# Kernel tuning notes

Hardware: AMD Instinct MI355X
Metric: run time of the kernel (lower is better)

## Reference

```python
import jax, jax.numpy as jnp
import numpy as np

KS = 5          # B-spline kernel_size per pseudo-coordinate dim
DIM = 2         # pseudo-coordinate dimensionality
NUM_GRAPHS = 64


def spline_conv(x, src, dst, edge_attr, W, root, bias):
    """Degree-1 open B-spline conv (torch-spline-conv semantics, aggr='mean').
    x: [N,Cin], edge_attr: [E,DIM] in [0,1], W: [KS**DIM,Cin,Cout]."""
    N = x.shape[0]
    E = src.shape[0]
    v = edge_attr * (KS - 1)                                   # [E,DIM]
    k_lo = jnp.clip(jnp.floor(v), 0, KS - 2).astype(jnp.int32) # lower knot index
    frac = v - k_lo.astype(v.dtype)                            # [E,DIM]
    # Precompute x @ W_k for all K kernel weights per node: [N,K,Cout]
    xW = jnp.einsum('nc,kco->nko', x, W)
    msg = jnp.zeros((E, W.shape[2]), x.dtype)
    # 2^DIM = 4 nonzero basis products for degree-1 splines
    for bits in ((0, 0), (0, 1), (1, 0), (1, 1)):
        b = jnp.ones((E,), x.dtype)
        wi = jnp.zeros((E,), jnp.int32)
        stride = 1
        for d, bit in enumerate(bits):
            b = b * (frac[:, d] if bit else (1.0 - frac[:, d]))
            wi = wi + (k_lo[:, d] + bit) * stride
            stride *= KS
        msg = msg + b[:, None] * xW[src, wi]                   # gather [E,Cout]
    agg = jax.ops.segment_sum(msg, dst, num_segments=N)
    deg = jax.ops.segment_sum(jnp.ones((E,), x.dtype), dst, num_segments=N)
    agg = agg / jnp.maximum(deg, 1.0)[:, None]                 # mean aggregation
    return agg + x @ root + bias


def setup_inputs() -> dict:
    key = jax.random.key(0)
    ks = jax.random.split(key, 12)
    N, E = 20000, 320000
    Cin, H, O = 1, 32, 10
    K = KS * KS
    p = lambda k, s: jax.random.normal(k, s, jnp.float32) * 0.1
    return {
        'x': jax.random.normal(ks[0], (N, Cin), jnp.float32),
        'edge_attr': jax.random.uniform(ks[1], (E, DIM), jnp.float32),
        'W1': p(ks[2], (K, Cin, H)), 'root1': p(ks[3], (Cin, H)), 'b1': jnp.zeros((H,), jnp.float32),
        'W2': p(ks[4], (K, H, 2 * H)), 'root2': p(ks[5], (H, 2 * H)), 'b2': jnp.zeros((2 * H,), jnp.float32),
        'Wf1': p(ks[6], (2 * H, 128)), 'bf1': jnp.zeros((128,), jnp.float32),
        'Wf2': p(ks[7], (128, O)), 'bf2': jnp.zeros((O,), jnp.float32),
        'edge_index': jax.random.randint(ks[8], (2, E), 0, N),
        'batch': jnp.sort(jax.random.randint(ks[9], (N,), 0, NUM_GRAPHS)),
    }


def reference(x, edge_attr, W1, root1, b1, W2, root2, b2, Wf1, bf1, Wf2, bf2, edge_index, batch):
    src, dst = edge_index[0], edge_index[1]
    h = jax.nn.relu(spline_conv(x, src, dst, edge_attr, W1, root1, b1))
    h = jax.nn.relu(spline_conv(h, src, dst, edge_attr, W2, root2, b2))
    # global mean pool over graphs
    gsum = jax.ops.segment_sum(h, batch, num_segments=NUM_GRAPHS)
    cnt = jax.ops.segment_sum(jnp.ones((h.shape[0],), h.dtype), batch, num_segments=NUM_GRAPHS)
    g = gsum / jnp.maximum(cnt, 1.0)[:, None]
    g = jax.nn.relu(g @ Wf1 + bf1)
    return jax.nn.log_softmax(g @ Wf2 + bf2, axis=1)
```

## Files before the change

### kernel.cpp

```cpp
#include <hip/hip_runtime.h>
#include <hip/hip_fp16.h>
#include <math.h>

#define KK 25
#define H1C 32
#define H2C 64
#define FCC 128
#define NCLS 10
#define NG 64
#define M1 16
#define M2 8
#define TILEU 12800

typedef _Float16 v8h __attribute__((ext_vector_type(8)));
typedef _Float16 v4h __attribute__((ext_vector_type(4)));
typedef float v4f __attribute__((ext_vector_type(4)));

__global__ __launch_bounds__(256) void deg_kernel(
    const int* __restrict__ edge_index, int E,
    int* __restrict__ degi,
    const float* __restrict__ W2, __half* __restrict__ W2t) {
    int i = blockIdx.x * 256 + threadIdx.x;
    if (i < KK * H2C * H1C) {
        int c = i & 31, o = (i >> 5) & 63, k = i >> 11;
        W2t[i] = __float2half(W2[(k * H1C + c) * H2C + o]);
    }
    if (i < E) atomicAdd(&degi[edge_index[E + i]], 1);
}

__global__ void scan1_kernel(const int* __restrict__ degi, int N,
                             int* __restrict__ incl, int* __restrict__ bsum) {
    __shared__ int s[256];
    int tid = threadIdx.x;
    int i = blockIdx.x * 256 + tid;
    int v = (i < N) ? degi[i] : 0;
    s[tid] = v;
    __syncthreads();
    for (int off = 1; off < 256; off <<= 1) {
        int t = (tid >= off) ? s[tid - off] : 0;
        __syncthreads();
        s[tid] += t;
        __syncthreads();
    }
    if (i < N) incl[i] = s[tid];
    if (tid == 255) bsum[blockIdx.x] = s[255];
}

__global__ void scan23_kernel(const int* __restrict__ incl, const int* __restrict__ degi,
                              const int* __restrict__ bsum, int nb, int N,
                              int* __restrict__ rowst, int* __restrict__ cur) {
    __shared__ int s[256];
    int tid = threadIdx.x;
    int lim = min(nb, (int)blockIdx.x);
    int v = 0;
    for (int j = tid; j < lim; j += 256) v += bsum[j];
    s[tid] = v;
    __syncthreads();
    for (int off = 1; off < 256; off <<= 1) {
        int t = (tid >= off) ? s[tid - off] : 0;
        __syncthreads();
        s[tid] += t;
        __syncthreads();
    }
    int prior = s[255];
    int i = blockIdx.x * 256 + tid;
    if (i < N) {
        int r = incl[i] - degi[i] + prior;
        rowst[i] = r;
        cur[i] = r;
    }
}

__global__ void bucket_kernel(const float* __restrict__ edge_attr,
                              const int* __restrict__ edge_index, int E,
                              int* __restrict__ cur, int4* __restrict__ es) {
    int e = blockIdx.x * blockDim.x + threadIdx.x;
    if (e >= E) return;
    float v0 = edge_attr[2 * e + 0] * 4.0f;
    float v1 = edge_attr[2 * e + 1] * 4.0f;
    int k0 = (int)floorf(v0); k0 = min(max(k0, 0), 3);
    int k1 = (int)floorf(v1); k1 = min(max(k1, 0), 3);
    float f0 = v0 - (float)k0, f1 = v1 - (float)k1;
    int dst = edge_index[E + e];
    int pos = atomicAdd(&cur[dst], 1);
    es[pos] = make_int4(edge_index[e], (dst << 8) | (k0 + 5 * k1),
                        __float_as_int(f0), __float_as_int(f1));
}

__global__ __launch_bounds__(256) void l1_kernel(
    const float* __restrict__ x,
    const int* __restrict__ rowst, const int* __restrict__ degi,
    const int4* __restrict__ es,
    const float* __restrict__ W1, const float* __restrict__ root1,
    const float* __restrict__ b1,
    const __half* __restrict__ W2t,
    int N, int E,
    float* __restrict__ h1, __half* __restrict__ xph) {
    __shared__ float w1s[KK * H1C];
    __shared__ float agg1[M1 * H1C];
    __shared__ int4 eb[8][32];
    __shared__ float xb[8][32];
    __shared__ __half h1s[M1][H1C];
    __shared__ __half stg[5][M1][68];
    int tid = threadIdx.x;
    for (int i = tid; i < KK * H1C; i += 256) w1s[i] = W1[i];
    for (int i = tid; i < M1 * H1C; i += 256) agg1[i] = 0.0f;
    __syncthreads();
    int g = tid >> 5, o = tid & 31;
    int n0 = blockIdx.x * M1;
    int blkBeg = rowst[n0];
    int blkEnd = (n0 + M1 < N) ? rowst[n0 + M1] : E;
    int total = blkEnd - blkBeg;
    int per = (total + 7) >> 3;
    int wBeg = blkBeg + g * per;
    int wEnd = min(blkEnd, wBeg + per);
    int curDst = -1;
    float acc = 0.0f;
    for (int base = wBeg; base < wEnd; base += 32) {
        int m = min(32, wEnd - base);
        if (o < m) {
            int4 ed = es[base + o];
            eb[g][o] = ed;
            xb[g][o] = x[ed.x];
        }
        for (int j = 0; j < m; j++) {
            int4 ed = eb[g][j];
            float xs = xb[g][j];
            int dst = ed.y >> 8;
            if (dst != curDst) {
                if (curDst >= 0) atomicAdd(&agg1[(curDst - n0) * H1C + o], acc);
                acc = 0.0f;
                curDst = dst;
            }
            float f0 = __int_as_float(ed.z), f1 = __int_as_float(ed.w);
            float g0 = 1.0f - f0, g1 = 1.0f - f1;
            int kb = (ed.y & 0xff) << 5;
            float coef = g0 * g1 * w1s[kb + o] + f0 * g1 * w1s[kb + 32 + o] +
                         g0 * f1 * w1s[kb + 160 + o] + f0 * f1 * w1s[kb + 192 + o];
            acc = fmaf(xs, coef, acc);
        }
    }
    if (curDst >= 0) atomicAdd(&agg1[(curDst - n0) * H1C + o], acc);
    __syncthreads();
#pragma unroll
    for (int i = 0; i < 2; i++) {
        int ln = g + 8 * i;
        int n = n0 + ln;
        if (n < N) {
            float rdeg = 1.0f / fmaxf((float)degi[n], 1.0f);
            float hv = fmaxf(agg1[ln * H1C + o] * rdeg + x[n] * root1[o] + b1[o], 0.0f);
            h1[n * H1C + o] = hv;
            h1s[ln][o] = __float2half(hv);
        } else {
            h1s[ln][o] = __float2half(0.0f);
        }
    }
    __syncthreads();

    int w = tid >> 6, lane = tid & 63;
    int r15 = lane & 15, quad = lane >> 4;
    int o0 = w * 16;
    v8h bfrag = *(const v8h*)(&h1s[r15][quad * 8]);
    __half* xtile = xph + (size_t)blockIdx.x * (2 * TILEU);
    int cln = tid >> 4, coc = (tid & 15) * 4;
    bool crow = (n0 + cln) < N;
    for (int kc = 0; kc < KK; kc += 5) {
#pragma unroll
        for (int kk = 0; kk < 5; kk++) {
            int k = kc + kk;
            v8h afrag = *(const v8h*)(W2t + ((k << 6) + o0 + r15) * H1C + quad * 8);
            v4f acc2 = {};
            acc2 = __builtin_amdgcn_mfma_f32_16x16x32_f16(afrag, bfrag, acc2, 0, 0, 0);
            v4h hv;
            hv[0] = (_Float16)acc2[0];
            hv[1] = (_Float16)acc2[1];
            hv[2] = (_Float16)acc2[2];
            hv[3] = (_Float16)acc2[3];
            *(v4h*)(&stg[kk][r15][o0 + quad * 4]) = hv;
        }
        __syncthreads();
#pragma unroll
        for (int kk = 0; kk < 5; kk++) {
            if (crow) {
                v4h hv = *(const v4h*)(&stg[kk][cln][coc]);
                *(v4h*)(xtile + ((kc + kk) << 10) + (tid << 2)) = hv;
            }
        }
        __syncthreads();
    }
}

__global__ __launch_bounds__(256) void l2_kernel(
    const float* __restrict__ h1,
    const int* __restrict__ rowst, const int* __restrict__ degi,
    const int4* __restrict__ es,
    const unsigned* __restrict__ xphu,
    const float* __restrict__ root2, const float* __restrict__ b2,
    const int* __restrict__ batch,
    int N, int E, float* __restrict__ gsum) {
    __shared__ float agg[M2 * H2C];
    __shared__ int4 eb[4][64];
    int tid = threadIdx.x;
    for (int i = tid; i < M2 * H2C; i += 256) agg[i] = 0.0f;
    __syncthreads();
    int w = tid >> 6, lane = tid & 63;
    int o2 = lane & 31, eh = lane >> 5;
    int n0 = blockIdx.x * M2;
    int blkBeg = rowst[n0];
    int blkEnd = (n0 + M2 < N) ? rowst[n0 + M2] : E;
    int total = blkEnd - blkBeg;
    int per = (total + 3) >> 2;
    int wBeg = blkBeg + w * per;
    int wEnd = min(blkEnd, wBeg + per);
    int curDst = -1;
    float ax = 0.0f, ay = 0.0f;
    for (int base = wBeg; base < wEnd; base += 64) {
        int m = min(64, wEnd - base);
        if (lane < m) eb[w][lane] = es[base + lane];
        for (int j = 0; j < m; j += 2) {
            int jj = j + eh;
            bool act = jj < m;
            int4 ed = eb[w][act ? jj : j];
            const unsigned* p = xphu + (size_t)(ed.x >> 4) * TILEU +
                                ((ed.y & 0xff) << 9) + ((ed.x & 15) << 5) + o2;
            unsigned t0 = p[0], t1 = p[512], t2 = p[2560], t3 = p[3072];
            if (act) {
                int dst = ed.y >> 8;
                if (dst != curDst) {
                    if (curDst >= 0) {
                        atomicAdd(&agg[(curDst - n0) * H2C + 2 * o2], ax);
                        atomicAdd(&agg[(curDst - n0) * H2C + 2 * o2 + 1], ay);
                    }
                    ax = ay = 0.0f;
                    curDst = dst;
                }
                float f0 = __int_as_float(ed.z), f1 = __int_as_float(ed.w);
                float g0 = 1.0f - f0, g1 = 1.0f - f1;
                float b0 = g0 * g1, b1 = f0 * g1, bb2 = g0 * f1, b3 = f0 * f1;
                __half2 h0 = *(__half2*)&t0, h1v = *(__half2*)&t1;
                __half2 h2 = *(__half2*)&t2, h3 = *(__half2*)&t3;
                ax = fmaf(b0, __low2float(h0), ax);  ay = fmaf(b0, __high2float(h0), ay);
                ax = fmaf(b1, __low2float(h1v), ax); ay = fmaf(b1, __high2float(h1v), ay);
                ax = fmaf(bb2, __low2float(h2), ax); ay = fmaf(bb2, __high2float(h2), ay);
                ax = fmaf(b3, __low2float(h3), ax);  ay = fmaf(b3, __high2float(h3), ay);
            }
        }
    }
    if (curDst >= 0) {
        atomicAdd(&agg[(curDst - n0) * H2C + 2 * o2], ax);
        atomicAdd(&agg[(curDst - n0) * H2C + 2 * o2 + 1], ay);
    }
    __syncthreads();

#pragma unroll
    for (int i = 0; i < 2; i++) {
        int ln = w + 4 * i;
        int n = n0 + ln;
        if (n < N) {
            float rd = 1.0f / fmaxf((float)degi[n], 1.0f);
            float v = agg[ln * H2C + lane] * rd + b2[lane];
            const float* hr = h1 + n * H1C;
#pragma unroll 8
            for (int c = 0; c < H1C; c++) v = fmaf(hr[c], root2[c * H2C + lane], v);
            agg[ln * H2C + lane] = fmaxf(v, 0.0f);
        } else {
            agg[ln * H2C + lane] = 0.0f;
        }
    }
    __syncthreads();

    if (tid < H2C) {
        float run = 0.0f;
        int curg = batch[n0];
        for (int ln = 0; ln < M2; ln++) {
            int n = n0 + ln;
            if (n >= N) break;
            int gg = batch[n];
            if (gg != curg) {
                atomicAdd(&gsum[curg * H2C + tid], run);
                run = 0.0f;
                curg = gg;
            }
            run += agg[ln * H2C + tid];
        }
        atomicAdd(&gsum[curg * H2C + tid], run);
    }
}

__global__ void head_kernel(const float* __restrict__ gsum,
                            const int* __restrict__ batch, int N,
                            const float* __restrict__ Wf1, const float* __restrict__ bf1,
                            const float* __restrict__ Wf2, const float* __restrict__ bf2,
                            float* __restrict__ out) {
    __shared__ float gc[H2C];
    __shared__ float t1[FCC];
    __shared__ float lg[NCLS];
    __shared__ float lse;
    __shared__ float scnt;
    int g = blockIdx.x, tid = threadIdx.x;
    if (tid == 0) {
        int lo = 0, hi = N;
        while (lo < hi) { int m = (lo + hi) >> 1; if (batch[m] < g) lo = m + 1; else hi = m; }
        int lb = lo;
        lo = 0; hi = N;
        while (lo < hi) { int m = (lo + hi) >> 1; if (batch[m] <= g) lo = m + 1; else hi = m; }
        scnt = (float)(lo - lb);
    }
    __syncthreads();
    if (tid < H2C) gc[tid] = gsum[g * H2C + tid] / fmaxf(scnt, 1.0f);
    __syncthreads();
    {
        float acc = bf1[tid];
        for (int c = 0; c < H2C; c++) acc += gc[c] * Wf1[c * FCC + tid];
        t1[tid] = fmaxf(acc, 0.0f);
    }
    __syncthreads();
    if (tid < NCLS) {
        float acc = bf2[tid];
        for (int j = 0; j < FCC; j++) acc += t1[j] * Wf2[j * NCLS + tid];
        lg[tid] = acc;
    }
    __syncthreads();
    if (tid == 0) {
        float m = lg[0];
        for (int c = 1; c < NCLS; c++) m = fmaxf(m, lg[c]);
        float s = 0.0f;
        for (int c = 0; c < NCLS; c++) s += expf(lg[c] - m);
        lse = m + logf(s);
    }
    __syncthreads();
    if (tid < NCLS) out[g * NCLS + tid] = lg[tid] - lse;
}

extern "C" void kernel_launch(void* const* d_in, const int* in_sizes, int n_in,
                              void* d_out, int out_size, void* d_ws, size_t ws_size,
                              hipStream_t stream) {
    const float* x          = (const float*)d_in[0];
    const float* edge_attr  = (const float*)d_in[1];
    const float* W1         = (const float*)d_in[2];
    const float* root1      = (const float*)d_in[3];
    const float* b1         = (const float*)d_in[4];
    const float* W2         = (const float*)d_in[5];
    const float* root2      = (const float*)d_in[6];
    const float* b2         = (const float*)d_in[7];
    const float* Wf1        = (const float*)d_in[8];
    const float* bf1        = (const float*)d_in[9];
    const float* Wf2        = (const float*)d_in[10];
    const float* bf2        = (const float*)d_in[11];
    const int*   edge_index = (const int*)d_in[12];
    const int*   batch      = (const int*)d_in[13];
    float* out = (float*)d_out;

    const int N = in_sizes[13];
    const int E = in_sizes[12] / 2;
    const int NB = (N + 255) / 256;
    const int NT1 = (N + M1 - 1) / M1;

    int4*     es   = (int4*)d_ws;
    unsigned* xphu = (unsigned*)(es + E);
    __half*   w2t  = (__half*)(xphu + (size_t)NT1 * TILEU);
    float* gsum  = (float*)(w2t + KK * H2C * H1C);
    int*   degi  = (int*)(gsum + NG * H2C);
    int*   rowst = degi + N;
    int*   cur   = rowst + N;
    int*   incl  = cur + N;
    int*   bsum  = incl + N;
    float* h1    = (float*)(bsum + 256);

    hipMemsetAsync(gsum, 0, (size_t)NG * H2C * sizeof(float) + (size_t)N * sizeof(int),
                   stream);

    int degBlocks = (E + 255) / 256;
    deg_kernel<<<degBlocks, 256, 0, stream>>>(edge_index, E, degi, W2, w2t);

    scan1_kernel<<<NB, 256, 0, stream>>>(degi, N, incl, bsum);
    scan23_kernel<<<NB, 256, 0, stream>>>(incl, degi, bsum, NB, N, rowst, cur);

    bucket_kernel<<<(E + 255) / 256, 256, 0, stream>>>(edge_attr, edge_index, E, cur, es);

    l1_kernel<<<NT1, 256, 0, stream>>>(
        x, rowst, degi, es, W1, root1, b1, w2t, N, E, h1, (__half*)xphu);

    l2_kernel<<<(N + M2 - 1) / M2, 256, 0, stream>>>(
        h1, rowst, degi, es, xphu, root2, b2, batch, N, E, gsum);

    head_kernel<<<NG, FCC, 0, stream>>>(gsum, batch, N, Wf1, bf1, Wf2, bf2, out);
}
```

Measured before the change: 198.5 us.

## Shrink layer-2 nodes per block and software-pipeline edge gathers

Cuts the number of destination nodes per block in the second conv kernel from 8 to 2, giving many more blocks and finer load balance, and adapts the epilogue so only the first M2 waves handle node finalisation. The edge loop now prefetches the next pair of edges' gathered xW values before doing the FMA on the current pair, so gather latency overlaps with compute. In exchange it uses more registers and launches more blocks, each with its own per-block overhead and gsum atomics.

```diff
diff --git a/kernel.cpp b/kernel.cpp
--- a/kernel.cpp
+++ b/kernel.cpp
@@ -9,7 +9,7 @@
 #define NCLS 10
 #define NG 64
 #define M1 16
-#define M2 8
+#define M2 2
 #define TILEU 12800
 
 typedef _Float16 v8h __attribute__((ext_vector_type(8)));
@@ -217,15 +217,21 @@
     for (int base = wBeg; base < wEnd; base += 64) {
         int m = min(64, wEnd - base);
         if (lane < m) eb[w][lane] = es[base + lane];
+        int4 edA = eb[w][min(eh, m - 1)];
+        const unsigned* pA = xphu + (size_t)(edA.x >> 4) * TILEU +
+                             ((edA.y & 0xff) << 9) + ((edA.x & 15) << 5) + o2;
+        unsigned a0 = pA[0], a1 = pA[512], a2 = pA[2560], a3 = pA[3072];
         for (int j = 0; j < m; j += 2) {
-            int jj = j + eh;
-            bool act = jj < m;
-            int4 ed = eb[w][act ? jj : j];
-            const unsigned* p = xphu + (size_t)(ed.x >> 4) * TILEU +
-                                ((ed.y & 0xff) << 9) + ((ed.x & 15) << 5) + o2;
-            unsigned t0 = p[0], t1 = p[512], t2 = p[2560], t3 = p[3072];
-            if (act) {
-                int dst = ed.y >> 8;
+            int4 edB = edA;
+            unsigned c0 = a0, c1 = a1, c2 = a2, c3 = a3;
+            if (j + 2 < m) {
+                edB = eb[w][min(j + 2 + eh, m - 1)];
+                const unsigned* pB = xphu + (size_t)(edB.x >> 4) * TILEU +
+                                     ((edB.y & 0xff) << 9) + ((edB.x & 15) << 5) + o2;
+                c0 = pB[0]; c1 = pB[512]; c2 = pB[2560]; c3 = pB[3072];
+            }
+            if (j + eh < m) {
+                int dst = edA.y >> 8;
                 if (dst != curDst) {
                     if (curDst >= 0) {
                         atomicAdd(&agg[(curDst - n0) * H2C + 2 * o2], ax);
@@ -234,16 +240,18 @@
                     ax = ay = 0.0f;
                     curDst = dst;
                 }
-                float f0 = __int_as_float(ed.z), f1 = __int_as_float(ed.w);
+                float f0 = __int_as_float(edA.z), f1 = __int_as_float(edA.w);
                 float g0 = 1.0f - f0, g1 = 1.0f - f1;
                 float b0 = g0 * g1, b1 = f0 * g1, bb2 = g0 * f1, b3 = f0 * f1;
-                __half2 h0 = *(__half2*)&t0, h1v = *(__half2*)&t1;
-                __half2 h2 = *(__half2*)&t2, h3 = *(__half2*)&t3;
+                __half2 h0 = *(__half2*)&a0, h1v = *(__half2*)&a1;
+                __half2 h2 = *(__half2*)&a2, h3 = *(__half2*)&a3;
                 ax = fmaf(b0, __low2float(h0), ax);  ay = fmaf(b0, __high2float(h0), ay);
                 ax = fmaf(b1, __low2float(h1v), ax); ay = fmaf(b1, __high2float(h1v), ay);
                 ax = fmaf(bb2, __low2float(h2), ax); ay = fmaf(bb2, __high2float(h2), ay);
                 ax = fmaf(b3, __low2float(h3), ax);  ay = fmaf(b3, __high2float(h3), ay);
             }
+            edA = edB;
+            a0 = c0; a1 = c1; a2 = c2; a3 = c3;
         }
     }
     if (curDst >= 0) {
@@ -252,19 +260,17 @@
     }
     __syncthreads();
 
-#pragma unroll
-    for (int i = 0; i < 2; i++) {
-        int ln = w + 4 * i;
-        int n = n0 + ln;
+    if (w < M2) {
+        int n = n0 + w;
         if (n < N) {
             float rd = 1.0f / fmaxf((float)degi[n], 1.0f);
-            float v = agg[ln * H2C + lane] * rd + b2[lane];
+            float v = agg[w * H2C + lane] * rd + b2[lane];
             const float* hr = h1 + n * H1C;
 #pragma unroll 8
             for (int c = 0; c < H1C; c++) v = fmaf(hr[c], root2[c * H2C + lane], v);
-            agg[ln * H2C + lane] = fmaxf(v, 0.0f);
+            agg[w * H2C + lane] = fmaxf(v, 0.0f);
         } else {
-            agg[ln * H2C + lane] = 0.0f;
+            agg[w * H2C + lane] = 0.0f;
         }
     }
     __syncthreads();
```

New measurement: 212.2 us. 6.9% more time.
